# Kernel optimization log

Hardware: AMD Instinct MI355X
Metric: run time of the kernel (lower is better)

## Reference

```python
import jax, jax.numpy as jnp
import numpy as np

C = 256
HEADS = 4
RADIUS = 2
LN_EPS = 1e-5


def setup_inputs() -> dict:
    key = jax.random.key(0)
    ks = jax.random.split(key, 8)
    s = 0.02
    return {
        "feat": jax.random.normal(ks[0], (8, C, 64, 64), dtype=jnp.float32),
        "in_w": jax.random.normal(ks[1], (3 * C, C), dtype=jnp.float32) * s,
        "in_b": jnp.zeros((3 * C,), dtype=jnp.float32),
        "out_w": jax.random.normal(ks[2], (C, C), dtype=jnp.float32) * s,
        "out_b": jnp.zeros((C,), dtype=jnp.float32),
        "proj_w": jax.random.normal(ks[3], (C, 4 * C), dtype=jnp.float32) * s,
        "proj_b": jnp.zeros((C,), dtype=jnp.float32),
        "ln_g": jnp.ones((C,), dtype=jnp.float32),
        "ln_b": jnp.zeros((C,), dtype=jnp.float32),
    }


def _spatial_mask(h, w, radius):
    yy, xx = jnp.meshgrid(jnp.arange(h), jnp.arange(w), indexing="ij")
    coords = jnp.stack([yy.ravel(), xx.ravel()], axis=-1).astype(jnp.float32)  # [N,2]
    dist = jnp.abs(coords[:, None, :] - coords[None, :, :]).sum(-1)  # Manhattan [N,N]
    return jnp.where(dist > radius, -jnp.inf, 0.0).astype(jnp.float32)


def _attend(qf, mf, mask, in_w, in_b, out_w, out_b, proj_w, proj_b, ln_g, ln_b):
    b, c, h, w = qf.shape
    n = h * w
    d = c // HEADS
    qt = qf.reshape(b, c, n).transpose(0, 2, 1)  # [B,N,C]
    mt = mf.reshape(b, c, n).transpose(0, 2, 1)
    q = qt @ in_w[:c].T + in_b[:c]
    k = mt @ in_w[c:2 * c].T + in_b[c:2 * c]
    v = mt @ in_w[2 * c:].T + in_b[2 * c:]
    # [B,H,N,D]
    q = q.reshape(b, n, HEADS, d).transpose(0, 2, 1, 3)
    k = k.reshape(b, n, HEADS, d).transpose(0, 2, 1, 3)
    v = v.reshape(b, n, HEADS, d).transpose(0, 2, 1, 3)
    scores = jnp.einsum("bhnd,bhmd->bhnm", q, k) / jnp.sqrt(jnp.float32(d)) + mask
    attn = jax.nn.softmax(scores, axis=-1)
    ctx = jnp.einsum("bhnm,bhmd->bhnd", attn, v)
    ctx = ctx.transpose(0, 2, 1, 3).reshape(b, n, c) @ out_w.T + out_b  # [B,N,C]
    asym = jnp.concatenate([qt, ctx, jnp.abs(qt - ctx), qt * ctx], axis=-1)
    y = asym @ proj_w.T + proj_b
    mu = y.mean(-1, keepdims=True)
    var = ((y - mu) ** 2).mean(-1, keepdims=True)
    y = (y - mu) / jnp.sqrt(var + LN_EPS) * ln_g + ln_b
    y = jax.nn.relu(y)
    return y.transpose(0, 2, 1).reshape(b, c, h, w)


def reference(feat, in_w, in_b, out_w, out_b, proj_w, proj_b, ln_g, ln_b):
    b, c, h, w = feat.shape
    mid = w // 2
    left = feat[:, :, :, :mid]
    right = feat[:, :, :, mid:]
    right_mirror = right[:, :, :, ::-1]
    left_mirror = left[:, :, :, ::-1]
    mask = _spatial_mask(h, mid, RADIUS)
    args = (mask, in_w, in_b, out_w, out_b, proj_w, proj_b, ln_g, ln_b)
    left_asym = _attend(left, right_mirror, *args)
    right_asym = _attend(right, left_mirror, *args)
    return jnp.concatenate([left_asym, right_asym], axis=-1)
```

## Files before the change

### kernel.cpp

```cpp
#include <hip/hip_runtime.h>
#include <hip/hip_bf16.h>


#define NTOK 32768

using bf16x8 = __attribute__((ext_vector_type(8))) short;
using f32x4  = __attribute__((ext_vector_type(4))) float;

__device__ __forceinline__ float b2f(short s) {
    unsigned u = ((unsigned)(unsigned short)s) << 16;
    union { unsigned u; float f; } c; c.u = u; return c.f;
}
__device__ __forceinline__ short f2b(float f) {
    __hip_bfloat16 h = __float2bfloat16(f);
    return *(short*)&h;
}
__device__ __forceinline__ void async_copy16(const void* g, void* l) {
    __builtin_amdgcn_global_load_lds(
        (const __attribute__((address_space(1))) unsigned int*)g,
        (__attribute__((address_space(3))) unsigned int*)l, 16, 0, 0);
}

__global__ __launch_bounds__(256) void prep_kernel(const float* __restrict__ feat,
                                                   const float* __restrict__ in_w,
                                                   const float* __restrict__ out_w,
                                                   const float* __restrict__ proj_w,
                                                   __hip_bfloat16* __restrict__ X,
                                                   __hip_bfloat16* __restrict__ wbf) {
    const int bid = blockIdx.x;
    const int tid = threadIdx.x;
    if (bid < 4096) {
        __shared__ float tile[32][68];
        const int b   = bid >> 9;
        const int rem = bid & 511;
        const int sp0 = (rem & 63) * 64;
        const int c0  = (rem >> 6) * 32;
        #pragma unroll
        for (int u = 0; u < 2; ++u) {
            const int idx = tid + u * 256;
            const int cl = idx >> 4;
            const int sq = (idx & 15) * 4;
            const float4 v = *(const float4*)(feat + ((size_t)(b * 256 + c0 + cl) << 12) + sp0 + sq);
            tile[cl][sq]     = v.x;
            tile[cl][sq + 1] = v.y;
            tile[cl][sq + 2] = v.z;
            tile[cl][sq + 3] = v.w;
        }
        __syncthreads();
        #pragma unroll
        for (int u = 0; u < 2; ++u) {
            const int idx = tid + u * 256;
            const int tok = idx >> 3;
            const int cq  = (idx & 7) * 4;
            short4 s;
            s.x = f2b(tile[cq][tok]);
            s.y = f2b(tile[cq + 1][tok]);
            s.z = f2b(tile[cq + 2][tok]);
            s.w = f2b(tile[cq + 3][tok]);
            *(short4*)(X + (size_t)(b * 4096 + sp0 + tok) * 256 + c0 + cq) = s;
        }
    } else {
        const int i4 = (bid - 4096) * 1024 + tid * 4;
        if (i4 < 196608) {
            const float4 v = *(const float4*)(in_w + i4);
            short4 s = {f2b(v.x), f2b(v.y), f2b(v.z), f2b(v.w)};
            *(short4*)(wbf + i4) = s;
        }
        if (i4 < 65536) {
            const float4 v = *(const float4*)(out_w + i4);
            short4 s = {f2b(v.x), f2b(v.y), f2b(v.z), f2b(v.w)};
            *(short4*)(wbf + 196608 + i4) = s;
        }
        if (i4 < 262144) {
            const float4 v = *(const float4*)(proj_w + i4);
            short4 s = {f2b(v.x), f2b(v.y), f2b(v.z), f2b(v.w)};
            *(short4*)(wbf + 262144 + i4) = s;
        }
    }
}

template <int KDIM, bool OUT_BF16>
__global__ __launch_bounds__(256) void mfma_gemm(const __hip_bfloat16* __restrict__ A,
                                                 const __hip_bfloat16* __restrict__ W,
                                                 const float* __restrict__ bias,
                                                 void* __restrict__ C, int Ntot) {
    __shared__ __align__(16) short As[128 * 64];
    __shared__ __align__(16) short Bs[128 * 64];
    const int tid = threadIdx.x;
    const int m0 = blockIdx.x * 128;
    const int n0 = blockIdx.y * 128;
    const int wave = tid >> 6, lane = tid & 63;
    const int wm = (wave >> 1) * 64;
    const int wn = (wave & 1) * 64;
    const int fm = lane & 15;
    const int fq = lane >> 4;

    f32x4 acc[4][4] = {};

    for (int k0 = 0; k0 < KDIM; k0 += 64) {
        #pragma unroll
        for (int v = 0; v < 4; ++v) {
            const int qb = v * 256 + wave * 64;
            const int q = qb + lane;
            const int r = q >> 3;
            const int cs = (q & 7) ^ (r & 7);
            async_copy16(A + (size_t)(m0 + r) * KDIM + k0 + cs * 8, &As[qb * 8]);
            async_copy16(W + (size_t)(n0 + r) * KDIM + k0 + cs * 8, &Bs[qb * 8]);
        }
        __syncthreads();
        #pragma unroll
        for (int kk = 0; kk < 2; ++kk) {
            bf16x8 af[4], bw[4];
            #pragma unroll
            for (int i = 0; i < 4; ++i) {
                const int row = wm + i * 16 + fm;
                af[i] = *(const bf16x8*)(&As[row * 64 + (((fq + kk * 4) ^ (fm & 7)) * 8)]);
            }
            #pragma unroll
            for (int j = 0; j < 4; ++j) {
                const int row = wn + j * 16 + fm;
                bw[j] = *(const bf16x8*)(&Bs[row * 64 + (((fq + kk * 4) ^ (fm & 7)) * 8)]);
            }
            #pragma unroll
            for (int i = 0; i < 4; ++i)
                #pragma unroll
                for (int j = 0; j < 4; ++j)
                    acc[i][j] = __builtin_amdgcn_mfma_f32_16x16x32_bf16(af[i], bw[j], acc[i][j], 0, 0, 0);
        }
        __syncthreads();
    }
    #pragma unroll
    for (int j = 0; j < 4; ++j) {
        const int col = n0 + wn + j * 16 + fm;
        const float bv = bias[col];
        #pragma unroll
        for (int i = 0; i < 4; ++i) {
            #pragma unroll
            for (int r = 0; r < 4; ++r) {
                const int row = m0 + wm + i * 16 + fq * 4 + r;
                const float v = acc[i][j][r] + bv;
                if (OUT_BF16)
                    ((__hip_bfloat16*)C)[(size_t)row * Ntot + col] = __float2bfloat16(v);
                else
                    ((float*)C)[(size_t)row * Ntot + col] = v;
            }
        }
    }
}

#define P0DY ((2u)|(2u<<3)|(2u<<6)|(2u<<9)|(2u<<12)|(1u<<15)|(1u<<18)|(1u<<21))
#define P0DX ((2u)|(1u<<3)|(3u<<6)|(0u<<9)|(4u<<12)|(2u<<15)|(1u<<18)|(3u<<21))
#define P1DY ((3u)|(3u<<3)|(3u<<6)|(0u<<9)|(4u<<12)|(2u<<15)|(2u<<18)|(2u<<21))
#define P1DX ((2u)|(1u<<3)|(3u<<6)|(2u<<9)|(2u<<12)|(2u<<15)|(2u<<18)|(2u<<21))

__global__ __launch_bounds__(256) void attn_kernel(const __hip_bfloat16* __restrict__ qkv,
                                                   __hip_bfloat16* __restrict__ ctx) {
    const int t = blockIdx.x * 4 + (threadIdx.x >> 6);
    const int lane = threadIdx.x & 63;
    const int n  = lane >> 3;
    const int cg = lane & 7;
    const int x6 = t & 63;
    const int yq = (t >> 6) & 63;
    const int b  = t >> 12;
    const int side = x6 >> 5;
    const int x = x6 & 31;

    bool valid[2];
    size_t kb[2];
    #pragma unroll
    for (int p = 0; p < 2; ++p) {
        const unsigned dyp = p ? P1DY : P0DY;
        const unsigned dxp = p ? P1DX : P0DX;
        const int sh = 3 * n;
        const int dy = (int)((dyp >> sh) & 7) - 2;
        const int dx = (int)((dxp >> sh) & 7) - 2;
        const int yy = yq + dy, xx = x + dx;
        valid[p] = (p == 0 || n < 5) && yy >= 0 && yy < 64 && xx >= 0 && xx < 32;
        const int xm = side ? (31 - xx) : (63 - xx);
        int tm = (b << 12) + (yy << 6) + xm;
        if (!valid[p]) tm = t;
        kb[p] = (size_t)tm * 768 + 256 + cg * 8;
    }
    const size_t qb = (size_t)t * 768 + cg * 8;
    const size_t ob = (size_t)t * 256;

    #pragma unroll
    for (int hp = 0; hp < 2; ++hp) {
        bf16x8 q8[2], k8[2][2], v8[2][2];
        #pragma unroll
        for (int hh = 0; hh < 2; ++hh) {
            const int h = hp * 2 + hh;
            q8[hh] = *(const bf16x8*)(qkv + qb + h * 64);
            #pragma unroll
            for (int p = 0; p < 2; ++p) {
                k8[hh][p] = *(const bf16x8*)(qkv + kb[p] + h * 64);
                v8[hh][p] = *(const bf16x8*)(qkv + kb[p] + h * 64 + 256);
            }
        }
        #pragma unroll
        for (int hh = 0; hh < 2; ++hh) {
            float sc[2];
            #pragma unroll
            for (int p = 0; p < 2; ++p) {
                float s = 0.f;
                #pragma unroll
                for (int j = 0; j < 8; ++j) s += b2f(q8[hh][j]) * b2f(k8[hh][p][j]);
                s += __shfl_xor(s, 1, 64);
                s += __shfl_xor(s, 2, 64);
                s += __shfl_xor(s, 4, 64);
                sc[p] = valid[p] ? s * 0.125f : -1e30f;
            }
            const float p0 = __expf(sc[0]);
            const float p1 = __expf(sc[1]);
            float l = p0 + p1;
            l += __shfl_xor(l, 8, 64);
            l += __shfl_xor(l, 16, 64);
            l += __shfl_xor(l, 32, 64);

            float o[8];
            #pragma unroll
            for (int j = 0; j < 8; ++j)
                o[j] = p0 * b2f(v8[hh][0][j]) + p1 * b2f(v8[hh][1][j]);
            float r4[4];
            #pragma unroll
            for (int i = 0; i < 4; ++i) {
                const float a = o[2 * i], bb = o[2 * i + 1];
                const float mine = (n & 1) ? bb : a;
                const float theirs = (n & 1) ? a : bb;
                r4[i] = mine + __shfl_xor(theirs, 8, 64);
            }
            float r2[2];
            #pragma unroll
            for (int i = 0; i < 2; ++i) {
                const float a = r4[2 * i], bb = r4[2 * i + 1];
                const float mine = (n & 2) ? bb : a;
                const float theirs = (n & 2) ? a : bb;
                r2[i] = mine + __shfl_xor(theirs, 16, 64);
            }
            float ov;
            {
                const float a = r2[0], bb = r2[1];
                const float mine = (n & 4) ? bb : a;
                const float theirs = (n & 4) ? a : bb;
                ov = mine + __shfl_xor(theirs, 32, 64);
            }
            const float rl = __builtin_amdgcn_rcpf(l);
            ctx[ob + (hp * 2 + hh) * 64 + cg * 8 + n] = __float2bfloat16(ov * rl);
        }
    }
}

__global__ __launch_bounds__(256) void proj_ln_fused(const __hip_bfloat16* __restrict__ X,
                                                     const __hip_bfloat16* __restrict__ CTX,
                                                     const __hip_bfloat16* __restrict__ W2,
                                                     const float* __restrict__ out_b,
                                                     const __hip_bfloat16* __restrict__ W,
                                                     const float* __restrict__ bias,
                                                     const float* __restrict__ ln_g,
                                                     const float* __restrict__ ln_b,
                                                     float* __restrict__ out) {
    __shared__ __align__(16) short smem[36864];
    __shared__ float mu_s[64], inv_s[64];
    short* c2s = smem;
    short* As  = smem + 16384;
    short* Bs  = smem + 20480;
    const int tid = threadIdx.x;
    const int m0 = blockIdx.x * 64;
    const int b = m0 >> 12, sp0 = m0 & 4095;
    const int wave = tid >> 6, lane = tid & 63;
    const int wn = wave * 64;
    const int fm = lane & 15;
    const int fq = lane >> 4;

    {
        f32x4 acc2[4][4] = {};
        for (int k0 = 0; k0 < 256; k0 += 64) {
            #pragma unroll
            for (int v = 0; v < 2; ++v) {
                const int qbu = v * 256 + wave * 64;
                const int q = qbu + lane;
                const int r = q >> 3;
                const int cs = (q & 7) ^ (r & 7);
                async_copy16(CTX + (size_t)(m0 + r) * 256 + k0 + cs * 8, &As[qbu * 8]);
            }
            #pragma unroll
            for (int v = 0; v < 8; ++v) {
                const int qbu = v * 256 + wave * 64;
                const int q = qbu + lane;
                const int r = q >> 3;
                const int cs = (q & 7) ^ (r & 7);
                async_copy16(W2 + (size_t)r * 256 + k0 + cs * 8, &Bs[qbu * 8]);
            }
            __syncthreads();
            #pragma unroll
            for (int kk = 0; kk < 2; ++kk) {
                bf16x8 af[4], bw[4];
                #pragma unroll
                for (int i = 0; i < 4; ++i) {
                    const int row = i * 16 + fm;
                    af[i] = *(const bf16x8*)(&As[row * 64 + (((fq + kk * 4) ^ (fm & 7)) * 8)]);
                }
                #pragma unroll
                for (int j = 0; j < 4; ++j) {
                    const int row = wn + j * 16 + fm;
                    bw[j] = *(const bf16x8*)(&Bs[row * 64 + (((fq + kk * 4) ^ (fm & 7)) * 8)]);
                }
                #pragma unroll
                for (int i = 0; i < 4; ++i)
                    #pragma unroll
                    for (int j = 0; j < 4; ++j)
                        acc2[i][j] = __builtin_amdgcn_mfma_f32_16x16x32_bf16(af[i], bw[j], acc2[i][j], 0, 0, 0);
            }
            __syncthreads();
        }
        #pragma unroll
        for (int j = 0; j < 4; ++j) {
            const int col = wn + j * 16 + fm;
            const float bv = out_b[col];
            const int jch = col >> 3, cl = col & 7;
            #pragma unroll
            for (int i = 0; i < 4; ++i)
                #pragma unroll
                for (int rr = 0; rr < 4; ++rr) {
                    const int row = i * 16 + fq * 4 + rr;
                    const int slot = (jch & 24) | ((jch & 7) ^ (row & 7));
                    c2s[row * 256 + slot * 8 + cl] = f2b(acc2[i][j][rr] + bv);
                }
        }
    }
    __syncthreads();

    f32x4 acc[4][4] = {};
    for (int k0 = 0; k0 < 1024; k0 += 64) {
        const int g = k0 >> 8;
        const int cb = k0 & 255;
        #pragma unroll
        for (int v = 0; v < 8; ++v) {
            const int qbu = v * 256 + wave * 64;
            const int q = qbu + lane;
            const int r = q >> 3;
            const int cs = (q & 7) ^ (r & 7);
            async_copy16(W + (size_t)r * 1024 + k0 + cs * 8, &Bs[qbu * 8]);
        }
        if (g == 0) {
            #pragma unroll
            for (int v = 0; v < 2; ++v) {
                const int qbu = v * 256 + wave * 64;
                const int q = qbu + lane;
                const int r = q >> 3;
                const int cs = (q & 7) ^ (r & 7);
                async_copy16(X + (size_t)(m0 + r) * 256 + cb + cs * 8, &As[qbu * 8]);
            }
        } else if (g >= 2) {
            #pragma unroll
            for (int v = 0; v < 2; ++v) {
                const int q = v * 256 + tid;
                const int r = q >> 3;
                const int cs = (q & 7) ^ (r & 7);
                int4 qraw = *(const int4*)(X + (size_t)(m0 + r) * 256 + cb + cs * 8);
                const int jch = (cb >> 3) + cs;
                const int slot = (jch & 24) | ((jch & 7) ^ (r & 7));
                int4 craw = *(const int4*)(&c2s[r * 256 + slot * 8]);
                const short* qs = (const short*)&qraw;
                const short* cw = (const short*)&craw;
                short tmp[8];
                #pragma unroll
                for (int j = 0; j < 8; ++j) {
                    const float qv = b2f(qs[j]), cv = b2f(cw[j]);
                    tmp[j] = f2b(g == 2 ? fabsf(qv - cv) : qv * cv);
                }
                *(int4*)(&As[q * 8]) = *(int4*)tmp;
            }
        }
        __syncthreads();
        #pragma unroll
        for (int kk = 0; kk < 2; ++kk) {
            bf16x8 af[4], bw[4];
            if (g == 1) {
                #pragma unroll
                for (int i = 0; i < 4; ++i) {
                    const int row = i * 16 + fm;
                    const int jch = (cb >> 3) + fq + kk * 4;
                    const int slot = (jch & 24) | ((jch & 7) ^ (row & 7));
                    af[i] = *(const bf16x8*)(&c2s[row * 256 + slot * 8]);
                }
            } else {
                #pragma unroll
                for (int i = 0; i < 4; ++i) {
                    const int row = i * 16 + fm;
                    af[i] = *(const bf16x8*)(&As[row * 64 + (((fq + kk * 4) ^ (fm & 7)) * 8)]);
                }
            }
            #pragma unroll
            for (int j = 0; j < 4; ++j) {
                const int row = wn + j * 16 + fm;
                bw[j] = *(const bf16x8*)(&Bs[row * 64 + (((fq + kk * 4) ^ (fm & 7)) * 8)]);
            }
            #pragma unroll
            for (int i = 0; i < 4; ++i)
                #pragma unroll
                for (int j = 0; j < 4; ++j)
                    acc[i][j] = __builtin_amdgcn_mfma_f32_16x16x32_bf16(af[i], bw[j], acc[i][j], 0, 0, 0);
        }
        __syncthreads();
    }
    short* ys = smem;
    #pragma unroll
    for (int j = 0; j < 4; ++j) {
        const int col = wn + j * 16 + fm;
        const float bv = bias[col];
        #pragma unroll
        for (int i = 0; i < 4; ++i)
            #pragma unroll
            for (int r = 0; r < 4; ++r)
                ys[(i * 16 + fq * 4 + r) * 266 + col] = f2b(acc[i][j][r] + bv);
    }
    __syncthreads();
    {
        const int tt = tid >> 2, seg = tid & 3;
        float s = 0.f, ss = 0.f;
        #pragma unroll
        for (int j = 0; j < 64; ++j) {
            const float v = b2f(ys[tt * 266 + seg * 64 + j]);
            s += v; ss += v * v;
        }
        s += __shfl_xor(s, 1, 64);  ss += __shfl_xor(ss, 1, 64);
        s += __shfl_xor(s, 2, 64);  ss += __shfl_xor(ss, 2, 64);
        if (seg == 0) {
            const float mu = s * (1.f / 256.f);
            const float var = ss * (1.f / 256.f) - mu * mu;
            mu_s[tt] = mu;
            inv_s[tt] = rsqrtf(var + 1e-5f);
        }
    }
    __syncthreads();
    {
        const int tl = tid & 63;
        const int j0 = tid >> 6;
        const float mu = mu_s[tl], inv = inv_s[tl];
        #pragma unroll
        for (int u = 0; u < 64; ++u) {
            const int j = j0 * 64 + u;
            const float v = (b2f(ys[tl * 266 + j]) - mu) * inv * ln_g[j] + ln_b[j];
            out[((size_t)(b * 256 + j) << 12) + sp0 + tl] = fmaxf(v, 0.f);
        }
    }
}

extern "C" void kernel_launch(void* const* d_in, const int* in_sizes, int n_in,
                              void* d_out, int out_size, void* d_ws, size_t ws_size,
                              hipStream_t stream) {
    (void)in_sizes; (void)n_in; (void)out_size; (void)ws_size;
    const float* feat   = (const float*)d_in[0];
    const float* in_w   = (const float*)d_in[1];
    const float* in_b   = (const float*)d_in[2];
    const float* out_w  = (const float*)d_in[3];
    const float* out_b  = (const float*)d_in[4];
    const float* proj_w = (const float*)d_in[5];
    const float* proj_b = (const float*)d_in[6];
    const float* ln_g   = (const float*)d_in[7];
    const float* ln_b   = (const float*)d_in[8];
    float* out = (float*)d_out;

    char* ws = (char*)d_ws;
    __hip_bfloat16* Xbf  = (__hip_bfloat16*)(ws);
    __hip_bfloat16* wbf  = (__hip_bfloat16*)(ws + (size_t)(16) * (1 << 20));
    __hip_bfloat16* qkv  = (__hip_bfloat16*)(ws + (size_t)(17) * (1 << 20));
    __hip_bfloat16* ctx  = (__hip_bfloat16*)(ws + (size_t)(65) * (1 << 20));
    __hip_bfloat16* in_wbf   = wbf;
    __hip_bfloat16* out_wbf  = wbf + 196608;
    __hip_bfloat16* proj_wbf = wbf + 262144;

    prep_kernel   <<<4352, 256, 0, stream>>>(feat, in_w, out_w, proj_w, Xbf, wbf);
    mfma_gemm<256, true><<<dim3(256, 6), 256, 0, stream>>>(Xbf, in_wbf, in_b, qkv, 768);
    attn_kernel   <<<NTOK / 4, 256, 0, stream>>>(qkv, ctx);
    proj_ln_fused <<<NTOK / 64, 256, 0, stream>>>(Xbf, ctx, out_wbf, out_b,
                                                  proj_wbf, proj_b, ln_g, ln_b, out);
}
```

Baseline: 185.7 us.

## Split proj_ln_fused across 8 waves with 2x4 warp tiling

Doubles the block size of the fused projection+LayerNorm kernel from 256 to 512 threads. Each wave now covers a 32x64 output sub-tile instead of 64x64, which halves accumulator registers per wave. Load and LN loops are redistributed over the extra threads. The aim is more waves in flight to hide latency, at the cost of more redundant B-fragment LDS reads per block and wider barriers.

```diff
diff --git a/kernel.cpp b/kernel.cpp
--- a/kernel.cpp
+++ b/kernel.cpp
@@ -250,15 +250,15 @@
     }
 }
 
-__global__ __launch_bounds__(256) void proj_ln_fused(const __hip_bfloat16* __restrict__ X,
-                                                     const __hip_bfloat16* __restrict__ CTX,
-                                                     const __hip_bfloat16* __restrict__ W2,
-                                                     const float* __restrict__ out_b,
-                                                     const __hip_bfloat16* __restrict__ W,
-                                                     const float* __restrict__ bias,
-                                                     const float* __restrict__ ln_g,
-                                                     const float* __restrict__ ln_b,
-                                                     float* __restrict__ out) {
+__global__ __launch_bounds__(512, 4) void proj_ln_fused(const __hip_bfloat16* __restrict__ X,
+                                                        const __hip_bfloat16* __restrict__ CTX,
+                                                        const __hip_bfloat16* __restrict__ W2,
+                                                        const float* __restrict__ out_b,
+                                                        const __hip_bfloat16* __restrict__ W,
+                                                        const float* __restrict__ bias,
+                                                        const float* __restrict__ ln_g,
+                                                        const float* __restrict__ ln_b,
+                                                        float* __restrict__ out) {
     __shared__ __align__(16) short smem[36864];
     __shared__ float mu_s[64], inv_s[64];
     short* c2s = smem;
@@ -268,36 +268,34 @@
     const int m0 = blockIdx.x * 64;
     const int b = m0 >> 12, sp0 = m0 & 4095;
     const int wave = tid >> 6, lane = tid & 63;
-    const int wn = wave * 64;
+    const int wmh = (wave >> 2) * 32;
+    const int wn  = (wave & 3) * 64;
     const int fm = lane & 15;
     const int fq = lane >> 4;
 
     {
-        f32x4 acc2[4][4] = {};
+        f32x4 acc2[2][4] = {};
         for (int k0 = 0; k0 < 256; k0 += 64) {
-            #pragma unroll
-            for (int v = 0; v < 2; ++v) {
-                const int qbu = v * 256 + wave * 64;
-                const int q = qbu + lane;
+            {
+                const int q = tid;
                 const int r = q >> 3;
                 const int cs = (q & 7) ^ (r & 7);
-                async_copy16(CTX + (size_t)(m0 + r) * 256 + k0 + cs * 8, &As[qbu * 8]);
-            }
-            #pragma unroll
-            for (int v = 0; v < 8; ++v) {
-                const int qbu = v * 256 + wave * 64;
-                const int q = qbu + lane;
+                async_copy16(CTX + (size_t)(m0 + r) * 256 + k0 + cs * 8, &As[(wave * 64) * 8]);
+            }
+            #pragma unroll
+            for (int v = 0; v < 4; ++v) {
+                const int q = v * 512 + tid;
                 const int r = q >> 3;
                 const int cs = (q & 7) ^ (r & 7);
-                async_copy16(W2 + (size_t)r * 256 + k0 + cs * 8, &Bs[qbu * 8]);
+                async_copy16(W2 + (size_t)r * 256 + k0 + cs * 8, &Bs[(v * 512 + wave * 64) * 8]);
             }
             __syncthreads();
             #pragma unroll
             for (int kk = 0; kk < 2; ++kk) {
-                bf16x8 af[4], bw[4];
-                #pragma unroll
-                for (int i = 0; i < 4; ++i) {
-                    const int row = i * 16 + fm;
+                bf16x8 af[2], bw[4];
+                #pragma unroll
+                for (int i = 0; i < 2; ++i) {
+                    const int row = wmh + i * 16 + fm;
                     af[i] = *(const bf16x8*)(&As[row * 64 + (((fq + kk * 4) ^ (fm & 7)) * 8)]);
                 }
                 #pragma unroll
@@ -306,7 +304,7 @@
                     bw[j] = *(const bf16x8*)(&Bs[row * 64 + (((fq + kk * 4) ^ (fm & 7)) * 8)]);
                 }
                 #pragma unroll
-                for (int i = 0; i < 4; ++i)
+                for (int i = 0; i < 2; ++i)
                     #pragma unroll
                     for (int j = 0; j < 4; ++j)
                         acc2[i][j] = __builtin_amdgcn_mfma_f32_16x16x32_bf16(af[i], bw[j], acc2[i][j], 0, 0, 0);
@@ -319,10 +317,10 @@
             const float bv = out_b[col];
             const int jch = col >> 3, cl = col & 7;
             #pragma unroll
-            for (int i = 0; i < 4; ++i)
+            for (int i = 0; i < 2; ++i)
                 #pragma unroll
                 for (int rr = 0; rr < 4; ++rr) {
-                    const int row = i * 16 + fq * 4 + rr;
+                    const int row = wmh + i * 16 + fq * 4 + rr;
                     const int slot = (jch & 24) | ((jch & 7) ^ (row & 7));
                     c2s[row * 256 + slot * 8 + cl] = f2b(acc2[i][j][rr] + bv);
                 }
@@ -330,64 +328,56 @@
     }
     __syncthreads();
 
-    f32x4 acc[4][4] = {};
+    f32x4 acc[2][4] = {};
     for (int k0 = 0; k0 < 1024; k0 += 64) {
         const int g = k0 >> 8;
         const int cb = k0 & 255;
         #pragma unroll
-        for (int v = 0; v < 8; ++v) {
-            const int qbu = v * 256 + wave * 64;
-            const int q = qbu + lane;
+        for (int v = 0; v < 4; ++v) {
+            const int q = v * 512 + tid;
             const int r = q >> 3;
             const int cs = (q & 7) ^ (r & 7);
-            async_copy16(W + (size_t)r * 1024 + k0 + cs * 8, &Bs[qbu * 8]);
+            async_copy16(W + (size_t)r * 1024 + k0 + cs * 8, &Bs[(v * 512 + wave * 64) * 8]);
         }
         if (g == 0) {
-            #pragma unroll
-            for (int v = 0; v < 2; ++v) {
-                const int qbu = v * 256 + wave * 64;
-                const int q = qbu + lane;
-                const int r = q >> 3;
-                const int cs = (q & 7) ^ (r & 7);
-                async_copy16(X + (size_t)(m0 + r) * 256 + cb + cs * 8, &As[qbu * 8]);
-            }
+            const int q = tid;
+            const int r = q >> 3;
+            const int cs = (q & 7) ^ (r & 7);
+            async_copy16(X + (size_t)(m0 + r) * 256 + cb + cs * 8, &As[(wave * 64) * 8]);
         } else if (g >= 2) {
-            #pragma unroll
-            for (int v = 0; v < 2; ++v) {
-                const int q = v * 256 + tid;
-                const int r = q >> 3;
-                const int cs = (q & 7) ^ (r & 7);
-                int4 qraw = *(const int4*)(X + (size_t)(m0 + r) * 256 + cb + cs * 8);
-                const int jch = (cb >> 3) + cs;
-                const int slot = (jch & 24) | ((jch & 7) ^ (r & 7));
-                int4 craw = *(const int4*)(&c2s[r * 256 + slot * 8]);
-                const short* qs = (const short*)&qraw;
-                const short* cw = (const short*)&craw;
-                short tmp[8];
-                #pragma unroll
-                for (int j = 0; j < 8; ++j) {
-                    const float qv = b2f(qs[j]), cv = b2f(cw[j]);
-                    tmp[j] = f2b(g == 2 ? fabsf(qv - cv) : qv * cv);
-                }
-                *(int4*)(&As[q * 8]) = *(int4*)tmp;
-            }
+            const int q = tid;
+            const int r = q >> 3;
+            const int cs = (q & 7) ^ (r & 7);
+            int4 qraw = *(const int4*)(X + (size_t)(m0 + r) * 256 + cb + cs * 8);
+            const int jch = (cb >> 3) + cs;
+            const int slot = (jch & 24) | ((jch & 7) ^ (r & 7));
+            int4 craw = *(const int4*)(&c2s[r * 256 + slot * 8]);
+            const short* qs = (const short*)&qraw;
+            const short* cw = (const short*)&craw;
+            short tmp[8];
+            #pragma unroll
+            for (int j = 0; j < 8; ++j) {
+                const float qv = b2f(qs[j]), cv = b2f(cw[j]);
+                tmp[j] = f2b(g == 2 ? fabsf(qv - cv) : qv * cv);
+            }
+            *(int4*)(&As[q * 8]) = *(int4*)tmp;
         }
         __syncthreads();
         #pragma unroll
         for (int kk = 0; kk < 2; ++kk) {
-            bf16x8 af[4], bw[4];
+            bf16x8 af[2], bw[4];
             if (g == 1) {
                 #pragma unroll
-                for (int i = 0; i < 4; ++i) {
-                    const int row = i * 16 + fm;
+                for (int i = 0; i < 2; ++i) {
+                    const int row = wmh + i * 16 + fm;
                     const int jch = (cb >> 3) + fq + kk * 4;
                     const int slot = (jch & 24) | ((jch & 7) ^ (row & 7));
                     af[i] = *(const bf16x8*)(&c2s[row * 256 + slot * 8]);
                 }
             } else {
                 #pragma unroll
-                for (int i = 0; i < 4; ++i) {
-                    const int row = i * 16 + fm;
+                for (int i = 0; i < 2; ++i) {
+                    const int row = wmh + i * 16 + fm;
                     af[i] = *(const bf16x8*)(&As[row * 64 + (((fq + kk * 4) ^ (fm & 7)) * 8)]);
                 }
             }
@@ -397,7 +387,7 @@
                 bw[j] = *(const bf16x8*)(&Bs[row * 64 + (((fq + kk * 4) ^ (fm & 7)) * 8)]);
             }
             #pragma unroll
-            for (int i = 0; i < 4; ++i)
+            for (int i = 0; i < 2; ++i)
                 #pragma unroll
                 for (int j = 0; j < 4; ++j)
                     acc[i][j] = __builtin_amdgcn_mfma_f32_16x16x32_bf16(af[i], bw[j], acc[i][j], 0, 0, 0);
@@ -410,22 +400,23 @@
         const int col = wn + j * 16 + fm;
         const float bv = bias[col];
         #pragma unroll
-        for (int i = 0; i < 4; ++i)
+        for (int i = 0; i < 2; ++i)
             #pragma unroll
             for (int r = 0; r < 4; ++r)
-                ys[(i * 16 + fq * 4 + r) * 266 + col] = f2b(acc[i][j][r] + bv);
+                ys[(wmh + i * 16 + fq * 4 + r) * 266 + col] = f2b(acc[i][j][r] + bv);
     }
     __syncthreads();
     {
-        const int tt = tid >> 2, seg = tid & 3;
+        const int tt = tid >> 3, seg = tid & 7;
         float s = 0.f, ss = 0.f;
         #pragma unroll
-        for (int j = 0; j < 64; ++j) {
-            const float v = b2f(ys[tt * 266 + seg * 64 + j]);
+        for (int j = 0; j < 32; ++j) {
+            const float v = b2f(ys[tt * 266 + seg * 32 + j]);
             s += v; ss += v * v;
         }
         s += __shfl_xor(s, 1, 64);  ss += __shfl_xor(ss, 1, 64);
         s += __shfl_xor(s, 2, 64);  ss += __shfl_xor(ss, 2, 64);
+        s += __shfl_xor(s, 4, 64);  ss += __shfl_xor(ss, 4, 64);
         if (seg == 0) {
             const float mu = s * (1.f / 256.f);
             const float var = ss * (1.f / 256.f) - mu * mu;
@@ -439,8 +430,8 @@
         const int j0 = tid >> 6;
         const float mu = mu_s[tl], inv = inv_s[tl];
         #pragma unroll
-        for (int u = 0; u < 64; ++u) {
-            const int j = j0 * 64 + u;
+        for (int u = 0; u < 32; ++u) {
+            const int j = j0 * 32 + u;
             const float v = (b2f(ys[tl * 266 + j]) - mu) * inv * ln_g[j] + ln_b[j];
             out[((size_t)(b * 256 + j) << 12) + sp0 + tl] = fmaxf(v, 0.f);
         }
@@ -474,6 +465,6 @@
     prep_kernel   <<<4352, 256, 0, stream>>>(feat, in_w, out_w, proj_w, Xbf, wbf);
     mfma_gemm<256, true><<<dim3(256, 6), 256, 0, stream>>>(Xbf, in_wbf, in_b, qkv, 768);
     attn_kernel   <<<NTOK / 4, 256, 0, stream>>>(qkv, ctx);
-    proj_ln_fused <<<NTOK / 64, 256, 0, stream>>>(Xbf, ctx, out_wbf, out_b,
+    proj_ln_fused <<<NTOK / 64, 512, 0, stream>>>(Xbf, ctx, out_wbf, out_b,
                                                   proj_wbf, proj_b, ln_g, ln_b, out);
 }
```

Measured after the change: 184.8 us. No clear change (-0.5%).
